# Performance work log

Hardware: AMD Instinct MI355X
Metric: run time of the kernel (lower is better)

The kernel has to match this reference:

```python
import jax, jax.numpy as jnp
import numpy as np

N_NODES = 100000
N_EDGES = 1600000
IN_CH = 32
HID = 128
OUT_CH = 32


def _glorot(key, shape):
    fan_in, fan_out = shape[1], shape[0]
    lim = (6.0 / (fan_in + fan_out)) ** 0.5
    return jax.random.uniform(key, shape, jnp.float32, -lim, lim)


def setup_inputs() -> dict:
    key = jax.random.key(0)
    ks = jax.random.split(key, 8)
    x = jax.random.normal(ks[0], (N_NODES, IN_CH), jnp.float32)
    edge_index = jax.random.randint(ks[1], (2, N_EDGES), 0, N_NODES, jnp.int64)
    # SAGEConv params: lin_l (neighbor agg, with bias), lin_r (root, no bias)
    W1_l = _glorot(ks[2], (HID, IN_CH))
    W1_r = _glorot(ks[3], (HID, IN_CH))
    b1 = jnp.zeros((HID,), jnp.float32)
    W2_l = _glorot(ks[4], (OUT_CH, HID))
    W2_r = _glorot(ks[5], (OUT_CH, HID))
    b2 = jnp.zeros((OUT_CH,), jnp.float32)
    return {"x": x, "edge_index": edge_index,
            "W1_l": W1_l, "W1_r": W1_r, "b1": b1,
            "W2_l": W2_l, "W2_r": W2_r, "b2": b2}


def _sage_conv(x, src, dst, W_l, W_r, b):
    # mean aggregation of neighbor features j -> i over edges (src=j, dst=i)
    agg = jax.ops.segment_sum(x[src], dst, num_segments=N_NODES)  # [N, C]
    deg = jax.ops.segment_sum(jnp.ones((src.shape[0],), x.dtype), dst,
                              num_segments=N_NODES)
    agg = agg / jnp.maximum(deg, 1.0)[:, None]
    return agg @ W_l.T + x @ W_r.T + b


def reference(x, edge_index, W1_l, W1_r, b1, W2_l, W2_r, b2):
    src, dst = edge_index[0], edge_index[1]
    h = _sage_conv(x, src, dst, W1_l, W1_r, b1)
    h = jax.nn.relu(h)
    # dropout is identity in eval mode (training=False)
    out = _sage_conv(h, src, dst, W2_l, W2_r, b2)
    return out
```

## Files before the change

kernel.cpp:

```cpp
#include <hip/hip_runtime.h>
#include <hip/hip_bf16.h>

typedef __hip_bfloat16 bf16;
typedef unsigned short ush;
typedef __attribute__((ext_vector_type(8))) unsigned short ush8;
typedef __attribute__((ext_vector_type(8))) short s8v;
typedef __attribute__((ext_vector_type(4))) float f4;

#define IN_CH 32
#define HID 128
#define OUT_CH 32
#define S_CAP 32
#define OVF_CAP 80000
#define NB_MAX 2048
#define SC_CHUNK 8192

__device__ __forceinline__ float bf2f(ush u) {
    return __uint_as_float(((unsigned)u) << 16);
}
__device__ __forceinline__ ush f2bf(float f) {
    __hip_bfloat16 b = __float2bfloat16(f);
    return __builtin_bit_cast(ush, b);
}
__device__ __forceinline__ float ldf(const void* __restrict__ p, size_t idx, int isbf16) {
    return isbf16 ? bf2f(((const ush*)p)[idx]) : ((const float*)p)[idx];
}
__device__ __forceinline__ int ld_edge(const int* __restrict__ ei, size_t elem, int wide) {
    return wide ? ei[2 * elem] : ei[elem];
}

__global__ void k_detect(const unsigned short* __restrict__ xraw,
                         const int* __restrict__ ei, int* __restrict__ flags) {
    __shared__ int cnt_exp, any_nz;
    if (threadIdx.x == 0) { cnt_exp = 0; any_nz = 0; }
    __syncthreads();
    int local = 0;
    for (int k = threadIdx.x; k < 4096; k += 256) {
        int e = (xraw[k] >> 7) & 0xFF;
        if (e >= 100 && e <= 140) ++local;
    }
    atomicAdd(&cnt_exp, local);
    for (int k = threadIdx.x; k < 2048; k += 256)
        if (ei[2 * k + 1] != 0) any_nz = 1;
    __syncthreads();
    if (threadIdx.x == 0) {
        flags[0] = (cnt_exp > 3500) ? 1 : 0;
        flags[1] = any_nz ? 0 : 1;
    }
}

__global__ void k_fillp(const int* __restrict__ ei, int n_edges,
                        const int* __restrict__ flags,
                        int* __restrict__ cnt, int* __restrict__ csr,
                        int* __restrict__ ovf, int* __restrict__ ovfn) {
    int e = blockIdx.x * blockDim.x + threadIdx.x;
    if (e >= n_edges) return;
    int w = flags[1];
    int d  = ld_edge(ei, (size_t)n_edges + e, w);
    int sc = ld_edge(ei, (size_t)e, w);
    int r = atomicAdd(&cnt[d], 1);
    if (r < S_CAP) {
        csr[d * S_CAP + r] = sc;
    } else {
        int o = atomicAdd(ovfn, 1);
        if (o < OVF_CAP) { ((int2*)ovf)[o] = make_int2(d, sc); }
    }
}


__global__ __launch_bounds__(256) void k_hist(
        const int* __restrict__ ei, int n_edges,
        const int* __restrict__ flags,
        int* __restrict__ hist, int NB) {
    __shared__ int hl[NB_MAX];
    int t = threadIdx.x;
    for (int k = t; k < NB; k += 256) hl[k] = 0;
    __syncthreads();
    int w = flags[1];
    int stride = gridDim.x * 256;
    for (int e = blockIdx.x * 256 + t; e < n_edges; e += stride) {
        int d = ld_edge(ei, (size_t)n_edges + e, w);
        atomicAdd(&hl[d >> 8], 1);
    }
    __syncthreads();
    for (int k = t; k < NB; k += 256)
        if (hl[k]) atomicAdd(&hist[k], hl[k]);
}

__global__ __launch_bounds__(256) void k_scan(
        const int* __restrict__ hist,
        int* __restrict__ base, int* __restrict__ cursor, int NB) {
    __shared__ int part[256];
    int t = threadIdx.x;
    int chunk = (NB + 255) / 256;
    int lo = t * chunk, hi = min(NB, (t + 1) * chunk);
    int s = 0;
    for (int k = lo; k < hi; ++k) s += hist[k];
    part[t] = s;
    __syncthreads();
    if (t == 0) {
        int r = 0;
        for (int q = 0; q < 256; ++q) { int v = part[q]; part[q] = r; r += v; }
        base[NB] = r;
    }
    __syncthreads();
    int r = part[t];
    for (int k = lo; k < hi; ++k) {
        base[k] = r; cursor[k] = r;
        r += hist[k];
    }
}

__global__ __launch_bounds__(256) void k_scatter(
        const int* __restrict__ ei, int n_edges,
        const int* __restrict__ flags,
        int* __restrict__ cursor, int* __restrict__ pairs, int NB) {
    __shared__ int cA[NB_MAX];
    __shared__ int oA[NB_MAX];
    int t = threadIdx.x;
    int w = flags[1];
    int e0 = blockIdx.x * SC_CHUNK;
    int ecnt = min(SC_CHUNK, n_edges - e0);
    if (ecnt <= 0) return;
    for (int k = t; k < NB; k += 256) cA[k] = 0;
    __syncthreads();
    for (int k = t; k < ecnt; k += 256) {
        int d = ld_edge(ei, (size_t)n_edges + e0 + k, w);
        atomicAdd(&cA[d >> 8], 1);
    }
    __syncthreads();
    for (int b = t; b < NB; b += 256) {
        int c = cA[b];
        oA[b] = c ? atomicAdd(&cursor[b], c) : 0;
        cA[b] = 0;
    }
    __syncthreads();
    for (int k = t; k < ecnt; k += 256) {
        int d  = ld_edge(ei, (size_t)n_edges + e0 + k, w);
        int sc = ld_edge(ei, (size_t)e0 + k, w);
        int b = d >> 8;
        int r = atomicAdd(&cA[b], 1);
        pairs[oA[b] + r] = sc | ((d & 255) << 24);
    }
}

__global__ __launch_bounds__(256) void k_build(
        const int* __restrict__ pairs, const int* __restrict__ base,
        int* __restrict__ cnt, int* __restrict__ csr,
        int* __restrict__ ovf, int* __restrict__ ovfn, int n_nodes) {
    __shared__ int cntL[256];
    __shared__ int im[256 * S_CAP];
    int b = blockIdx.x;
    int t = threadIdx.x;
    cntL[t] = 0;
    __syncthreads();
    int s0 = base[b], s1 = base[b + 1];
    int node0 = b << 8;
    for (int k = s0 + t; k < s1; k += 256) {
        int v = pairs[k];
        int src = v & 0x00FFFFFF;
        int ld = ((unsigned)v) >> 24;
        int r = atomicAdd(&cntL[ld], 1);
        if (r < S_CAP) {
            im[ld * S_CAP + r] = src;
        } else {
            int o = atomicAdd(ovfn, 1);
            if (o < OVF_CAP) { ((int2*)ovf)[o] = make_int2(node0 + ld, src); }
        }
    }
    __syncthreads();
    int nvalid = min(256, n_nodes - node0);
    if (t < nvalid) cnt[node0 + t] = cntL[t];
    for (int k = t; k < nvalid * S_CAP; k += 256)
        csr[(size_t)node0 * S_CAP + k] = im[k];
}

__global__ __launch_bounds__(256, 8) void k_agg1(
        const void* __restrict__ x,
        const int* __restrict__ cnt, const int* __restrict__ csr,
        const int* __restrict__ ovf, const int* __restrict__ ovfn,
        const int* __restrict__ flags,
        float* __restrict__ aggf, ush* __restrict__ aggb, int aggf32,
        int n_nodes) {
    int fb = flags[0];
    int t = threadIdx.x;
    int wave = t >> 6, lane = t & 63;
    int slot = lane >> 2;
    int chunk = lane & 3;
    int st = gridDim.x * 4 * 2;
    int i = (blockIdx.x * 4 + wave) * 2;
    if (i >= n_nodes) return;
    int idxv = csr[(size_t)i * S_CAP + lane];
    int dgv  = cnt[min(i + (lane & 1), n_nodes - 1)];
    while (i < n_nodes) {
        int inext = i + st;
        int idxv_n = 0, dgv_n = 0;
        if (inext < n_nodes) {
            idxv_n = csr[(size_t)inext * S_CAP + lane];
            dgv_n  = cnt[min(inext + (lane & 1), n_nodes - 1)];
        }
        int dg0 = __shfl(dgv, 0);
        int dg1 = __shfl(dgv, 1);
        bool has1 = (i + 1) < n_nodes;
        int lim0 = min(dg0, S_CAP);
        int lim1 = has1 ? min(dg1, S_CAP) : 0;
        int lmax = max(lim0, lim1);
        float acc0[8] = {0, 0, 0, 0, 0, 0, 0, 0};
        float acc1[8] = {0, 0, 0, 0, 0, 0, 0, 0};
        if (fb) {
            const ush* xb = (const ush*)x;
            for (int g = 0; g < lmax; g += 16) {
                int k = g + slot;
                int s0 = __shfl(idxv, k);
                int s1 = __shfl(idxv, 32 + k);
                bool ok0 = k < lim0;
                bool ok1 = k < lim1;
                ush8 v0 = *(const ush8*)(xb + (size_t)(ok0 ? s0 : i) * IN_CH + chunk * 8);
                ush8 v1 = *(const ush8*)(xb + (size_t)(ok1 ? s1 : i) * IN_CH + chunk * 8);
#pragma unroll
                for (int j = 0; j < 8; ++j) {
                    acc0[j] += ok0 ? bf2f(v0[j]) : 0.0f;
                    acc1[j] += ok1 ? bf2f(v1[j]) : 0.0f;
                }
            }
            if (dg0 > S_CAP) {
                int on = min(*ovfn, OVF_CAP);
                for (int k = 0; k < on; ++k) {
                    int2 pr = ((const int2*)ovf)[k];
                    if (pr.x == i && slot == 0) {
                        ush8 v = *(const ush8*)(xb + (size_t)pr.y * IN_CH + chunk * 8);
#pragma unroll
                        for (int j = 0; j < 8; ++j) acc0[j] += bf2f(v[j]);
                    }
                }
            }
            if (has1 && dg1 > S_CAP) {
                int on = min(*ovfn, OVF_CAP);
                for (int k = 0; k < on; ++k) {
                    int2 pr = ((const int2*)ovf)[k];
                    if (pr.x == i + 1 && slot == 0) {
                        ush8 v = *(const ush8*)(xb + (size_t)pr.y * IN_CH + chunk * 8);
#pragma unroll
                        for (int j = 0; j < 8; ++j) acc1[j] += bf2f(v[j]);
                    }
                }
            }
        } else {
            const float* xb = (const float*)x;
            for (int g = 0; g < lmax; g += 16) {
                int k = g + slot;
                int s0 = __shfl(idxv, k);
                int s1 = __shfl(idxv, 32 + k);
                bool ok0 = k < lim0;
                bool ok1 = k < lim1;
                const float* r0 = xb + (size_t)(ok0 ? s0 : i) * IN_CH + chunk * 8;
                const float* r1 = xb + (size_t)(ok1 ? s1 : i) * IN_CH + chunk * 8;
                f4 a0 = *(const f4*)r0;
                f4 a1 = *(const f4*)(r0 + 4);
                f4 b0 = *(const f4*)r1;
                f4 b1 = *(const f4*)(r1 + 4);
#pragma unroll
                for (int j = 0; j < 4; ++j) {
                    acc0[j]     += ok0 ? a0[j] : 0.0f;
                    acc0[4 + j] += ok0 ? a1[j] : 0.0f;
                    acc1[j]     += ok1 ? b0[j] : 0.0f;
                    acc1[4 + j] += ok1 ? b1[j] : 0.0f;
                }
            }
            if (dg0 > S_CAP) {
                int on = min(*ovfn, OVF_CAP);
                for (int k = 0; k < on; ++k) {
                    int2 pr = ((const int2*)ovf)[k];
                    if (pr.x == i && slot == 0) {
                        const float* rp = xb + (size_t)pr.y * IN_CH + chunk * 8;
                        f4 a0 = *(const f4*)rp;
                        f4 a1 = *(const f4*)(rp + 4);
#pragma unroll
                        for (int j = 0; j < 4; ++j) { acc0[j] += a0[j]; acc0[4 + j] += a1[j]; }
                    }
                }
            }
            if (has1 && dg1 > S_CAP) {
                int on = min(*ovfn, OVF_CAP);
                for (int k = 0; k < on; ++k) {
                    int2 pr = ((const int2*)ovf)[k];
                    if (pr.x == i + 1 && slot == 0) {
                        const float* rp = xb + (size_t)pr.y * IN_CH + chunk * 8;
                        f4 a0 = *(const f4*)rp;
                        f4 a1 = *(const f4*)(rp + 4);
#pragma unroll
                        for (int j = 0; j < 4; ++j) { acc1[j] += a0[j]; acc1[4 + j] += a1[j]; }
                    }
                }
            }
        }
#pragma unroll
        for (int j = 0; j < 8; ++j) {
            acc0[j] += __shfl_xor(acc0[j], 4);
            acc0[j] += __shfl_xor(acc0[j], 8);
            acc0[j] += __shfl_xor(acc0[j], 16);
            acc0[j] += __shfl_xor(acc0[j], 32);
            acc1[j] += __shfl_xor(acc1[j], 4);
            acc1[j] += __shfl_xor(acc1[j], 8);
            acc1[j] += __shfl_xor(acc1[j], 16);
            acc1[j] += __shfl_xor(acc1[j], 32);
        }
        if (lane < 8) {
            bool second = lane >= 4;
            if (!second || has1) {
                int node = second ? i + 1 : i;
                int dg = second ? dg1 : dg0;
                float rd = 1.0f / (float)(dg > 1 ? dg : 1);
                int c = lane & 3;
                float o[8];
#pragma unroll
                for (int j = 0; j < 8; ++j)
                    o[j] = (second ? acc1[j] : acc0[j]) * rd;
                if (aggf32) {
                    float* op = aggf + (size_t)node * IN_CH + c * 8;
                    f4 o0, o1;
#pragma unroll
                    for (int j = 0; j < 4; ++j) { o0[j] = o[j]; o1[j] = o[4 + j]; }
                    *(f4*)op = o0;
                    *(f4*)(op + 4) = o1;
                } else {
                    ush8 ov;
#pragma unroll
                    for (int j = 0; j < 8; ++j) ov[j] = f2bf(o[j]);
                    *(ush8*)(aggb + (size_t)node * IN_CH + c * 8) = ov;
                }
            }
        }
        i = inext; idxv = idxv_n; dgv = dgv_n;
    }
}

__global__ __launch_bounds__(256, 4) void k_mm1_mfma(
        const void* __restrict__ x,
        const float* __restrict__ aggf, const ush* __restrict__ aggb, int aggf32,
        const void* __restrict__ W1l, const void* __restrict__ W1r,
        const void* __restrict__ b1,
        const int* __restrict__ flags,
        ush* __restrict__ hout, int n_nodes) {
    __shared__ ush wst[HID * 64];
    int fb = flags[0];
    int t = threadIdx.x;
    for (int idx = t; idx < HID * IN_CH; idx += 256) {
        int o = idx >> 5, c = idx & 31;
        wst[o * 64 + c]      = f2bf(ldf(W1l, idx, fb));
        wst[o * 64 + 32 + c] = f2bf(ldf(W1r, idx, fb));
    }
    __syncthreads();
    int wave = t >> 6, lane = t & 63;
    int col  = lane & 15;
    int kgrp = lane >> 4;
    s8v bfr[8][2];
    float bias[8];
#pragma unroll
    for (int tt = 0; tt < 8; ++tt) {
        int o = tt * 16 + col;
#pragma unroll
        for (int q = 0; q < 2; ++q)
            bfr[tt][q] = __builtin_bit_cast(s8v, *(const ush8*)&wst[o * 64 + q * 32 + kgrp * 8]);
        bias[tt] = ldf(b1, o, fb);
    }
    int gw = blockIdx.x * 4 + wave;
    int nw = gridDim.x * 4;
    for (int n0 = gw * 16; n0 < n_nodes; n0 += nw * 16) {
        int arow = n0 + col;
        if (arow >= n_nodes) arow = n_nodes - 1;
        s8v a0;
        if (aggf32) {
            const float* ap = aggf + (size_t)arow * IN_CH + kgrp * 8;
            f4 v0 = *(const f4*)ap;
            f4 v1 = *(const f4*)(ap + 4);
            ush8 tmp;
#pragma unroll
            for (int j = 0; j < 4; ++j) { tmp[j] = f2bf(v0[j]); tmp[4 + j] = f2bf(v1[j]); }
            a0 = __builtin_bit_cast(s8v, tmp);
        } else {
            a0 = __builtin_bit_cast(s8v, *(const ush8*)(aggb + (size_t)arow * IN_CH + kgrp * 8));
        }
        s8v a1;
        if (fb) {
            a1 = __builtin_bit_cast(s8v, *(const ush8*)((const ush*)x + (size_t)arow * IN_CH + kgrp * 8));
        } else {
            const float* rp = (const float*)x + (size_t)arow * IN_CH + kgrp * 8;
            f4 v0 = *(const f4*)rp;
            f4 v1 = *(const f4*)(rp + 4);
            ush8 tmp;
#pragma unroll
            for (int j = 0; j < 4; ++j) { tmp[j] = f2bf(v0[j]); tmp[4 + j] = f2bf(v1[j]); }
            a1 = __builtin_bit_cast(s8v, tmp);
        }
        f4 acc[8];
#pragma unroll
        for (int tt = 0; tt < 8; ++tt) {
            f4 z = {0, 0, 0, 0};
            z = __builtin_amdgcn_mfma_f32_16x16x32_bf16(a0, bfr[tt][0], z, 0, 0, 0);
            z = __builtin_amdgcn_mfma_f32_16x16x32_bf16(a1, bfr[tt][1], z, 0, 0, 0);
            acc[tt] = z;
        }
#pragma unroll
        for (int r = 0; r < 4; ++r) {
            int node = n0 + kgrp * 4 + r;
            if (node < n_nodes) {
#pragma unroll
                for (int tt = 0; tt < 8; ++tt) {
                    float v = acc[tt][r] + bias[tt];
                    hout[(size_t)node * HID + tt * 16 + col] = f2bf(v > 0.0f ? v : 0.0f);
                }
            }
        }
    }
}

__global__ __launch_bounds__(256, 4) void k_g_mfma(
        ush* __restrict__ h, ush* __restrict__ gout,
        const void* __restrict__ W2l, const void* __restrict__ W2r,
        const void* __restrict__ b2,
        const int* __restrict__ flags, int n_nodes) {
    __shared__ ush wst[2 * OUT_CH * HID];
    int fb = flags[0];
    int t = threadIdx.x;
    for (int idx = t; idx < OUT_CH * HID; idx += 256) {
        wst[idx]                  = f2bf(ldf(W2l, idx, fb));
        wst[OUT_CH * HID + idx]   = f2bf(ldf(W2r, idx, fb));
    }
    __syncthreads();
    int wave = t >> 6, lane = t & 63;
    int col  = lane & 15;
    int kgrp = lane >> 4;
    s8v bfr[4][4];
#pragma unroll
    for (int tt = 0; tt < 4; ++tt) {
        int base = (tt < 2 ? 0 : OUT_CH * HID) + ((tt & 1) * 16 + col) * HID + kgrp * 8;
#pragma unroll
        for (int q = 0; q < 4; ++q)
            bfr[tt][q] = __builtin_bit_cast(s8v, *(const ush8*)&wst[base + q * 32]);
    }
    float bias0 = ldf(b2, col, fb);
    float bias1 = ldf(b2, 16 + col, fb);
    int gw = blockIdx.x * 4 + wave;
    int nw = gridDim.x * 4;
    for (int n0 = gw * 16; n0 < n_nodes; n0 += nw * 16) {
        int arow = n0 + col;
        if (arow >= n_nodes) arow = n_nodes - 1;
        const ush* hp = h + (size_t)arow * HID + kgrp * 8;
        s8v a0 = __builtin_bit_cast(s8v, *(const ush8*)(hp));
        s8v a1 = __builtin_bit_cast(s8v, *(const ush8*)(hp + 32));
        s8v a2 = __builtin_bit_cast(s8v, *(const ush8*)(hp + 64));
        s8v a3 = __builtin_bit_cast(s8v, *(const ush8*)(hp + 96));
        f4 acc0 = {0, 0, 0, 0}, acc1 = {0, 0, 0, 0}, acc2 = {0, 0, 0, 0}, acc3 = {0, 0, 0, 0};
        acc0 = __builtin_amdgcn_mfma_f32_16x16x32_bf16(a0, bfr[0][0], acc0, 0, 0, 0);
        acc0 = __builtin_amdgcn_mfma_f32_16x16x32_bf16(a1, bfr[0][1], acc0, 0, 0, 0);
        acc0 = __builtin_amdgcn_mfma_f32_16x16x32_bf16(a2, bfr[0][2], acc0, 0, 0, 0);
        acc0 = __builtin_amdgcn_mfma_f32_16x16x32_bf16(a3, bfr[0][3], acc0, 0, 0, 0);
        acc1 = __builtin_amdgcn_mfma_f32_16x16x32_bf16(a0, bfr[1][0], acc1, 0, 0, 0);
        acc1 = __builtin_amdgcn_mfma_f32_16x16x32_bf16(a1, bfr[1][1], acc1, 0, 0, 0);
        acc1 = __builtin_amdgcn_mfma_f32_16x16x32_bf16(a2, bfr[1][2], acc1, 0, 0, 0);
        acc1 = __builtin_amdgcn_mfma_f32_16x16x32_bf16(a3, bfr[1][3], acc1, 0, 0, 0);
        acc2 = __builtin_amdgcn_mfma_f32_16x16x32_bf16(a0, bfr[2][0], acc2, 0, 0, 0);
        acc2 = __builtin_amdgcn_mfma_f32_16x16x32_bf16(a1, bfr[2][1], acc2, 0, 0, 0);
        acc2 = __builtin_amdgcn_mfma_f32_16x16x32_bf16(a2, bfr[2][2], acc2, 0, 0, 0);
        acc2 = __builtin_amdgcn_mfma_f32_16x16x32_bf16(a3, bfr[2][3], acc2, 0, 0, 0);
        acc3 = __builtin_amdgcn_mfma_f32_16x16x32_bf16(a0, bfr[3][0], acc3, 0, 0, 0);
        acc3 = __builtin_amdgcn_mfma_f32_16x16x32_bf16(a1, bfr[3][1], acc3, 0, 0, 0);
        acc3 = __builtin_amdgcn_mfma_f32_16x16x32_bf16(a2, bfr[3][2], acc3, 0, 0, 0);
        acc3 = __builtin_amdgcn_mfma_f32_16x16x32_bf16(a3, bfr[3][3], acc3, 0, 0, 0);
#pragma unroll
        for (int r = 0; r < 4; ++r) {
            int node = n0 + kgrp * 4 + r;
            if (node < n_nodes) {
                gout[(size_t)node * OUT_CH + col]      = f2bf(acc0[r]);
                gout[(size_t)node * OUT_CH + 16 + col] = f2bf(acc1[r]);
                h[(size_t)node * HID + 32 + col]       = f2bf(acc2[r] + bias0);
                h[(size_t)node * HID + 48 + col]       = f2bf(acc3[r] + bias1);
            }
        }
    }
}

__global__ __launch_bounds__(256, 8) void k_l2g(
        const ush* __restrict__ gbuf, const ush* __restrict__ hs,
        const int* __restrict__ cnt, const int* __restrict__ csr,
        const int* __restrict__ ovf, const int* __restrict__ ovfn,
        const int* __restrict__ flags,
        void* __restrict__ out, int n_nodes) {
    int fb = flags[0];
    int t = threadIdx.x;
    int wave = t >> 6, lane = t & 63;
    int slot = lane >> 2;
    int chunk = lane & 3;
    int st = gridDim.x * 4 * 2;
    int i = (blockIdx.x * 4 + wave) * 2;
    if (i >= n_nodes) return;
    int idxv = csr[(size_t)i * S_CAP + lane];
    int dgv  = cnt[min(i + (lane & 1), n_nodes - 1)];
    while (i < n_nodes) {
        int inext = i + st;
        int idxv_n = 0, dgv_n = 0;
        if (inext < n_nodes) {
            idxv_n = csr[(size_t)inext * S_CAP + lane];
            dgv_n  = cnt[min(inext + (lane & 1), n_nodes - 1)];
        }
        int dg0 = __shfl(dgv, 0);
        int dg1 = __shfl(dgv, 1);
        bool has1 = (i + 1) < n_nodes;
        int lim0 = min(dg0, S_CAP);
        int lim1 = has1 ? min(dg1, S_CAP) : 0;
        int lmax = max(lim0, lim1);
        float acc0[8] = {0, 0, 0, 0, 0, 0, 0, 0};
        float acc1[8] = {0, 0, 0, 0, 0, 0, 0, 0};
        for (int g = 0; g < lmax; g += 16) {
            int k = g + slot;
            int s0 = __shfl(idxv, k);
            int s1 = __shfl(idxv, 32 + k);
            bool ok0 = k < lim0;
            bool ok1 = k < lim1;
            ush8 v0 = *(const ush8*)(gbuf + (size_t)(ok0 ? s0 : i) * OUT_CH + chunk * 8);
            ush8 v1 = *(const ush8*)(gbuf + (size_t)(ok1 ? s1 : i) * OUT_CH + chunk * 8);
#pragma unroll
            for (int j = 0; j < 8; ++j) {
                acc0[j] += ok0 ? bf2f(v0[j]) : 0.0f;
                acc1[j] += ok1 ? bf2f(v1[j]) : 0.0f;
            }
        }
        if (dg0 > S_CAP) {
            int on = min(*ovfn, OVF_CAP);
            for (int k = 0; k < on; ++k) {
                int2 pr = ((const int2*)ovf)[k];
                if (pr.x == i && slot == 0) {
                    ush8 v = *(const ush8*)(gbuf + (size_t)pr.y * OUT_CH + chunk * 8);
#pragma unroll
                    for (int j = 0; j < 8; ++j) acc0[j] += bf2f(v[j]);
                }
            }
        }
        if (has1 && dg1 > S_CAP) {
            int on = min(*ovfn, OVF_CAP);
            for (int k = 0; k < on; ++k) {
                int2 pr = ((const int2*)ovf)[k];
                if (pr.x == i + 1 && slot == 0) {
                    ush8 v = *(const ush8*)(gbuf + (size_t)pr.y * OUT_CH + chunk * 8);
#pragma unroll
                    for (int j = 0; j < 8; ++j) acc1[j] += bf2f(v[j]);
                }
            }
        }
#pragma unroll
        for (int j = 0; j < 8; ++j) {
            acc0[j] += __shfl_xor(acc0[j], 4);
            acc0[j] += __shfl_xor(acc0[j], 8);
            acc0[j] += __shfl_xor(acc0[j], 16);
            acc0[j] += __shfl_xor(acc0[j], 32);
            acc1[j] += __shfl_xor(acc1[j], 4);
            acc1[j] += __shfl_xor(acc1[j], 8);
            acc1[j] += __shfl_xor(acc1[j], 16);
            acc1[j] += __shfl_xor(acc1[j], 32);
        }
        if (lane < 8) {
            bool second = lane >= 4;
            if (!second || has1) {
                int node = second ? i + 1 : i;
                int dg = second ? dg1 : dg0;
                float rd = 1.0f / (float)(dg > 1 ? dg : 1);
                int c = lane & 3;
                ush8 selfv = *(const ush8*)(hs + (size_t)node * HID + 32 + c * 8);
                if (fb) {
                    ush8 ov;
#pragma unroll
                    for (int j = 0; j < 8; ++j) {
                        float a = second ? acc1[j] : acc0[j];
                        ov[j] = f2bf(a * rd + bf2f(selfv[j]));
                    }
                    *(ush8*)((ush*)out + (size_t)node * OUT_CH + c * 8) = ov;
                } else {
                    float* op = (float*)out + (size_t)node * OUT_CH + c * 8;
                    f4 a0, a1;
#pragma unroll
                    for (int j = 0; j < 4; ++j) {
                        float x0 = second ? acc1[j]     : acc0[j];
                        float x1 = second ? acc1[4 + j] : acc0[4 + j];
                        a0[j] = x0 * rd + bf2f(selfv[j]);
                        a1[j] = x1 * rd + bf2f(selfv[4 + j]);
                    }
                    *(f4*)op = a0;
                    *(f4*)(op + 4) = a1;
                }
            }
        }
        i = inext; idxv = idxv_n; dgv = dgv_n;
    }
}

extern "C" void kernel_launch(void* const* d_in, const int* in_sizes, int n_in,
                              void* d_out, int out_size, void* d_ws, size_t ws_size,
                              hipStream_t stream) {
    const void* x   = d_in[0];
    const int*  ei  = (const int*)d_in[1];
    const void* W1l = d_in[2];
    const void* W1r = d_in[3];
    const void* b1  = d_in[4];
    const void* W2l = d_in[5];
    const void* W2r = d_in[6];
    const void* b2  = d_in[7];

    int n_nodes = in_sizes[0] / IN_CH;
    int n_edges = in_sizes[1] / 2;

    char* ws = (char*)d_ws;
    size_t o_cnt = 256;
    size_t o_csr = (o_cnt + (size_t)n_nodes * 4 + 127) & ~(size_t)127;
    size_t o_ovf = (o_csr + ((size_t)n_nodes * S_CAP + 64) * 4 + 127) & ~(size_t)127;
    size_t o_hist = o_ovf + (size_t)OVF_CAP * 8;
    size_t o_h   = (o_hist + (size_t)(3 * (NB_MAX + 2)) * 4 + 255) & ~(size_t)255;
    size_t o_gb  = (o_h + (size_t)n_nodes * HID * 2 + 255) & ~(size_t)255;
    size_t o_ag  = (o_gb + (size_t)n_nodes * OUT_CH * 2 + 255) & ~(size_t)255;
    size_t need_f32 = o_ag + (size_t)n_nodes * IN_CH * 4;

    int* flags = (int*)ws;
    int* ovfn  = (int*)(ws + 128);
    int* cnt   = (int*)(ws + o_cnt);
    int* csr   = (int*)(ws + o_csr);
    int* ovf   = (int*)(ws + o_ovf);
    int* hist  = (int*)(ws + o_hist);
    int* base  = hist + NB_MAX;
    int* curs  = base + NB_MAX + 1;
    ush* h     = (ush*)(ws + o_h);
    int* pairs = (int*)(ws + o_h);
    ush* gbuf  = (ush*)(ws + o_gb);

    int aggf32 = (ws_size >= need_f32) ? 1 : 0;
    float* aggf = (float*)(ws + o_ag);
    ush*   aggb = gbuf;

    int NB = (n_nodes + 255) >> 8;
    int use_bucket = (NB <= NB_MAX) && (n_nodes < (1 << 24)) &&
                     ((size_t)n_edges * 4 <= (size_t)n_nodes * HID * 2) && (n_edges > 0);

    hipMemsetAsync(ws, 0, 256, stream);

    k_detect<<<1, 256, 0, stream>>>((const unsigned short*)x, ei, flags);

    if (use_bucket) {
        hipMemsetAsync(hist, 0, (size_t)NB * 4, stream);
        int nchunks = (n_edges + SC_CHUNK - 1) / SC_CHUNK;
        k_hist<<<256, 256, 0, stream>>>(ei, n_edges, flags, hist, NB);
        k_scan<<<1, 256, 0, stream>>>(hist, base, curs, NB);
        k_scatter<<<nchunks, 256, 0, stream>>>(ei, n_edges, flags, curs, pairs, NB);
        k_build<<<NB, 256, 0, stream>>>(pairs, base, cnt, csr, ovf, ovfn, n_nodes);
    } else {
        hipMemsetAsync(cnt, 0, (size_t)n_nodes * 4, stream);
        k_fillp<<<(n_edges + 255) / 256, 256, 0, stream>>>(ei, n_edges, flags, cnt, csr, ovf, ovfn);
    }

    k_agg1<<<2048, 256, 0, stream>>>(x, cnt, csr, ovf, ovfn, flags, aggf, aggb, aggf32, n_nodes);
    k_mm1_mfma<<<1024, 256, 0, stream>>>(x, aggf, aggb, aggf32, W1l, W1r, b1, flags, h, n_nodes);
    k_g_mfma<<<1024, 256, 0, stream>>>(h, gbuf, W2l, W2r, b2, flags, n_nodes);
    k_l2g<<<2048, 256, 0, stream>>>(gbuf, h, cnt, csr, ovf, ovfn, flags, d_out, n_nodes);
}
```

Baseline: 268.6 us.

## Remap gather kernels to one node per 4-lane group, sixteen nodes per wave

Both neighbour-gather kernels (layer-1 aggregation and layer-2 aggregation) now give each 4-lane group its own node instead of spreading two nodes' 32 neighbour slots across the whole wave. Each lane loads 8 CSR indices with vector loads, and lanes trade them with shuffles, so the cross-lane reduction tree over 16 slots is gone. The grid becomes one thread per node chunk instead of a grid-stride loop. This removes many shuffles and the masked-slot waste, but each wave now walks up to the largest degree among its 16 nodes sequentially, and the overflow scan runs per lane.

```diff
diff --git a/kernel.cpp b/kernel.cpp
--- a/kernel.cpp
+++ b/kernel.cpp
@@ -185,153 +185,96 @@
     int fb = flags[0];
     int t = threadIdx.x;
     int wave = t >> 6, lane = t & 63;
-    int slot = lane >> 2;
-    int chunk = lane & 3;
-    int st = gridDim.x * 4 * 2;
-    int i = (blockIdx.x * 4 + wave) * 2;
-    if (i >= n_nodes) return;
-    int idxv = csr[(size_t)i * S_CAP + lane];
-    int dgv  = cnt[min(i + (lane & 1), n_nodes - 1)];
-    while (i < n_nodes) {
-        int inext = i + st;
-        int idxv_n = 0, dgv_n = 0;
-        if (inext < n_nodes) {
-            idxv_n = csr[(size_t)inext * S_CAP + lane];
-            dgv_n  = cnt[min(inext + (lane & 1), n_nodes - 1)];
-        }
-        int dg0 = __shfl(dgv, 0);
-        int dg1 = __shfl(dgv, 1);
-        bool has1 = (i + 1) < n_nodes;
-        int lim0 = min(dg0, S_CAP);
-        int lim1 = has1 ? min(dg1, S_CAP) : 0;
-        int lmax = max(lim0, lim1);
-        float acc0[8] = {0, 0, 0, 0, 0, 0, 0, 0};
-        float acc1[8] = {0, 0, 0, 0, 0, 0, 0, 0};
-        if (fb) {
-            const ush* xb = (const ush*)x;
-            for (int g = 0; g < lmax; g += 16) {
-                int k = g + slot;
-                int s0 = __shfl(idxv, k);
-                int s1 = __shfl(idxv, 32 + k);
-                bool ok0 = k < lim0;
-                bool ok1 = k < lim1;
-                ush8 v0 = *(const ush8*)(xb + (size_t)(ok0 ? s0 : i) * IN_CH + chunk * 8);
-                ush8 v1 = *(const ush8*)(xb + (size_t)(ok1 ? s1 : i) * IN_CH + chunk * 8);
-#pragma unroll
-                for (int j = 0; j < 8; ++j) {
-                    acc0[j] += ok0 ? bf2f(v0[j]) : 0.0f;
-                    acc1[j] += ok1 ? bf2f(v1[j]) : 0.0f;
+    int g4 = lane & 60;
+    int c  = lane & 3;
+    int node = (blockIdx.x * 4 + wave) * 16 + (lane >> 2);
+    bool valid = node < n_nodes;
+    int nd = valid ? node : n_nodes - 1;
+    int dg = cnt[nd];
+    int lim = min(dg, S_CAP);
+    int idxr[8];
+    {
+        int4 i0 = *(const int4*)&csr[(size_t)nd * S_CAP + c * 8];
+        int4 i1 = *(const int4*)&csr[(size_t)nd * S_CAP + c * 8 + 4];
+        idxr[0] = i0.x; idxr[1] = i0.y; idxr[2] = i0.z; idxr[3] = i0.w;
+        idxr[4] = i1.x; idxr[5] = i1.y; idxr[6] = i1.z; idxr[7] = i1.w;
+    }
+    int lmax = lim;
+    lmax = max(lmax, __shfl_xor(lmax, 4));
+    lmax = max(lmax, __shfl_xor(lmax, 8));
+    lmax = max(lmax, __shfl_xor(lmax, 16));
+    lmax = max(lmax, __shfl_xor(lmax, 32));
+    float acc[8] = {0, 0, 0, 0, 0, 0, 0, 0};
+    if (fb) {
+        const ush* xb = (const ush*)x;
+        for (int kb = 0; kb < 4; ++kb) {
+            if (kb * 8 >= lmax) break;
+#pragma unroll
+            for (int kk = 0; kk < 8; ++kk) {
+                int src = __shfl(idxr[kk], g4 + kb);
+                if (kb * 8 + kk < lim) {
+                    ush8 v = *(const ush8*)(xb + (size_t)src * IN_CH + c * 8);
+#pragma unroll
+                    for (int j = 0; j < 8; ++j) acc[j] += bf2f(v[j]);
                 }
             }
-            if (dg0 > S_CAP) {
-                int on = min(*ovfn, OVF_CAP);
-                for (int k = 0; k < on; ++k) {
-                    int2 pr = ((const int2*)ovf)[k];
-                    if (pr.x == i && slot == 0) {
-                        ush8 v = *(const ush8*)(xb + (size_t)pr.y * IN_CH + chunk * 8);
-#pragma unroll
-                        for (int j = 0; j < 8; ++j) acc0[j] += bf2f(v[j]);
-                    }
+        }
+        if (dg > S_CAP) {
+            int on = min(*ovfn, OVF_CAP);
+            for (int k = 0; k < on; ++k) {
+                int2 pr = ((const int2*)ovf)[k];
+                if (pr.x == nd && valid) {
+                    ush8 v = *(const ush8*)(xb + (size_t)pr.y * IN_CH + c * 8);
+#pragma unroll
+                    for (int j = 0; j < 8; ++j) acc[j] += bf2f(v[j]);
                 }
             }
-            if (has1 && dg1 > S_CAP) {
-                int on = min(*ovfn, OVF_CAP);
-                for (int k = 0; k < on; ++k) {
-                    int2 pr = ((const int2*)ovf)[k];
-                    if (pr.x == i + 1 && slot == 0) {
-                        ush8 v = *(const ush8*)(xb + (size_t)pr.y * IN_CH + chunk * 8);
-#pragma unroll
-                        for (int j = 0; j < 8; ++j) acc1[j] += bf2f(v[j]);
-                    }
+        }
+    } else {
+        const float* xb = (const float*)x;
+        for (int kb = 0; kb < 4; ++kb) {
+            if (kb * 8 >= lmax) break;
+#pragma unroll
+            for (int kk = 0; kk < 8; ++kk) {
+                int src = __shfl(idxr[kk], g4 + kb);
+                if (kb * 8 + kk < lim) {
+                    const float* rp = xb + (size_t)src * IN_CH + c * 8;
+                    f4 a0 = *(const f4*)rp;
+                    f4 a1 = *(const f4*)(rp + 4);
+#pragma unroll
+                    for (int j = 0; j < 4; ++j) { acc[j] += a0[j]; acc[4 + j] += a1[j]; }
                 }
             }
+        }
+        if (dg > S_CAP) {
+            int on = min(*ovfn, OVF_CAP);
+            for (int k = 0; k < on; ++k) {
+                int2 pr = ((const int2*)ovf)[k];
+                if (pr.x == nd && valid) {
+                    const float* rp = xb + (size_t)pr.y * IN_CH + c * 8;
+                    f4 a0 = *(const f4*)rp;
+                    f4 a1 = *(const f4*)(rp + 4);
+#pragma unroll
+                    for (int j = 0; j < 4; ++j) { acc[j] += a0[j]; acc[4 + j] += a1[j]; }
+                }
+            }
+        }
+    }
+    if (valid) {
+        float rd = 1.0f / (float)(dg > 1 ? dg : 1);
+        if (aggf32) {
+            float* op = aggf + (size_t)node * IN_CH + c * 8;
+            f4 o0, o1;
+#pragma unroll
+            for (int j = 0; j < 4; ++j) { o0[j] = acc[j] * rd; o1[j] = acc[4 + j] * rd; }
+            *(f4*)op = o0;
+            *(f4*)(op + 4) = o1;
         } else {
-            const float* xb = (const float*)x;
-            for (int g = 0; g < lmax; g += 16) {
-                int k = g + slot;
-                int s0 = __shfl(idxv, k);
-                int s1 = __shfl(idxv, 32 + k);
-                bool ok0 = k < lim0;
-                bool ok1 = k < lim1;
-                const float* r0 = xb + (size_t)(ok0 ? s0 : i) * IN_CH + chunk * 8;
-                const float* r1 = xb + (size_t)(ok1 ? s1 : i) * IN_CH + chunk * 8;
-                f4 a0 = *(const f4*)r0;
-                f4 a1 = *(const f4*)(r0 + 4);
-                f4 b0 = *(const f4*)r1;
-                f4 b1 = *(const f4*)(r1 + 4);
-#pragma unroll
-                for (int j = 0; j < 4; ++j) {
-                    acc0[j]     += ok0 ? a0[j] : 0.0f;
-                    acc0[4 + j] += ok0 ? a1[j] : 0.0f;
-                    acc1[j]     += ok1 ? b0[j] : 0.0f;
-                    acc1[4 + j] += ok1 ? b1[j] : 0.0f;
-                }
-            }
-            if (dg0 > S_CAP) {
-                int on = min(*ovfn, OVF_CAP);
-                for (int k = 0; k < on; ++k) {
-                    int2 pr = ((const int2*)ovf)[k];
-                    if (pr.x == i && slot == 0) {
-                        const float* rp = xb + (size_t)pr.y * IN_CH + chunk * 8;
-                        f4 a0 = *(const f4*)rp;
-                        f4 a1 = *(const f4*)(rp + 4);
-#pragma unroll
-                        for (int j = 0; j < 4; ++j) { acc0[j] += a0[j]; acc0[4 + j] += a1[j]; }
-                    }
-                }
-            }
-            if (has1 && dg1 > S_CAP) {
-                int on = min(*ovfn, OVF_CAP);
-                for (int k = 0; k < on; ++k) {
-                    int2 pr = ((const int2*)ovf)[k];
-                    if (pr.x == i + 1 && slot == 0) {
-                        const float* rp = xb + (size_t)pr.y * IN_CH + chunk * 8;
-                        f4 a0 = *(const f4*)rp;
-                        f4 a1 = *(const f4*)(rp + 4);
-#pragma unroll
-                        for (int j = 0; j < 4; ++j) { acc1[j] += a0[j]; acc1[4 + j] += a1[j]; }
-                    }
-                }
-            }
-        }
-#pragma unroll
-        for (int j = 0; j < 8; ++j) {
-            acc0[j] += __shfl_xor(acc0[j], 4);
-            acc0[j] += __shfl_xor(acc0[j], 8);
-            acc0[j] += __shfl_xor(acc0[j], 16);
-            acc0[j] += __shfl_xor(acc0[j], 32);
-            acc1[j] += __shfl_xor(acc1[j], 4);
-            acc1[j] += __shfl_xor(acc1[j], 8);
-            acc1[j] += __shfl_xor(acc1[j], 16);
-            acc1[j] += __shfl_xor(acc1[j], 32);
-        }
-        if (lane < 8) {
-            bool second = lane >= 4;
-            if (!second || has1) {
-                int node = second ? i + 1 : i;
-                int dg = second ? dg1 : dg0;
-                float rd = 1.0f / (float)(dg > 1 ? dg : 1);
-                int c = lane & 3;
-                float o[8];
-#pragma unroll
-                for (int j = 0; j < 8; ++j)
-                    o[j] = (second ? acc1[j] : acc0[j]) * rd;
-                if (aggf32) {
-                    float* op = aggf + (size_t)node * IN_CH + c * 8;
-                    f4 o0, o1;
-#pragma unroll
-                    for (int j = 0; j < 4; ++j) { o0[j] = o[j]; o1[j] = o[4 + j]; }
-                    *(f4*)op = o0;
-                    *(f4*)(op + 4) = o1;
-                } else {
-                    ush8 ov;
-#pragma unroll
-                    for (int j = 0; j < 8; ++j) ov[j] = f2bf(o[j]);
-                    *(ush8*)(aggb + (size_t)node * IN_CH + c * 8) = ov;
-                }
-            }
-        }
-        i = inext; idxv = idxv_n; dgv = dgv_n;
+            ush8 ov;
+#pragma unroll
+            for (int j = 0; j < 8; ++j) ov[j] = f2bf(acc[j] * rd);
+            *(ush8*)(aggb + (size_t)node * IN_CH + c * 8) = ov;
+        }
     }
 }
 
@@ -490,107 +433,69 @@
     int fb = flags[0];
     int t = threadIdx.x;
     int wave = t >> 6, lane = t & 63;
-    int slot = lane >> 2;
-    int chunk = lane & 3;
-    int st = gridDim.x * 4 * 2;
-    int i = (blockIdx.x * 4 + wave) * 2;
-    if (i >= n_nodes) return;
-    int idxv = csr[(size_t)i * S_CAP + lane];
-    int dgv  = cnt[min(i + (lane & 1), n_nodes - 1)];
-    while (i < n_nodes) {
-        int inext = i + st;
-        int idxv_n = 0, dgv_n = 0;
-        if (inext < n_nodes) {
-            idxv_n = csr[(size_t)inext * S_CAP + lane];
-            dgv_n  = cnt[min(inext + (lane & 1), n_nodes - 1)];
-        }
-        int dg0 = __shfl(dgv, 0);
-        int dg1 = __shfl(dgv, 1);
-        bool has1 = (i + 1) < n_nodes;
-        int lim0 = min(dg0, S_CAP);
-        int lim1 = has1 ? min(dg1, S_CAP) : 0;
-        int lmax = max(lim0, lim1);
-        float acc0[8] = {0, 0, 0, 0, 0, 0, 0, 0};
-        float acc1[8] = {0, 0, 0, 0, 0, 0, 0, 0};
-        for (int g = 0; g < lmax; g += 16) {
-            int k = g + slot;
-            int s0 = __shfl(idxv, k);
-            int s1 = __shfl(idxv, 32 + k);
-            bool ok0 = k < lim0;
-            bool ok1 = k < lim1;
-            ush8 v0 = *(const ush8*)(gbuf + (size_t)(ok0 ? s0 : i) * OUT_CH + chunk * 8);
-            ush8 v1 = *(const ush8*)(gbuf + (size_t)(ok1 ? s1 : i) * OUT_CH + chunk * 8);
-#pragma unroll
-            for (int j = 0; j < 8; ++j) {
-                acc0[j] += ok0 ? bf2f(v0[j]) : 0.0f;
-                acc1[j] += ok1 ? bf2f(v1[j]) : 0.0f;
-            }
-        }
-        if (dg0 > S_CAP) {
-            int on = min(*ovfn, OVF_CAP);
-            for (int k = 0; k < on; ++k) {
-                int2 pr = ((const int2*)ovf)[k];
-                if (pr.x == i && slot == 0) {
-                    ush8 v = *(const ush8*)(gbuf + (size_t)pr.y * OUT_CH + chunk * 8);
-#pragma unroll
-                    for (int j = 0; j < 8; ++j) acc0[j] += bf2f(v[j]);
-                }
-            }
-        }
-        if (has1 && dg1 > S_CAP) {
-            int on = min(*ovfn, OVF_CAP);
-            for (int k = 0; k < on; ++k) {
-                int2 pr = ((const int2*)ovf)[k];
-                if (pr.x == i + 1 && slot == 0) {
-                    ush8 v = *(const ush8*)(gbuf + (size_t)pr.y * OUT_CH + chunk * 8);
-#pragma unroll
-                    for (int j = 0; j < 8; ++j) acc1[j] += bf2f(v[j]);
-                }
-            }
-        }
-#pragma unroll
-        for (int j = 0; j < 8; ++j) {
-            acc0[j] += __shfl_xor(acc0[j], 4);
-            acc0[j] += __shfl_xor(acc0[j], 8);
-            acc0[j] += __shfl_xor(acc0[j], 16);
-            acc0[j] += __shfl_xor(acc0[j], 32);
-            acc1[j] += __shfl_xor(acc1[j], 4);
-            acc1[j] += __shfl_xor(acc1[j], 8);
-            acc1[j] += __shfl_xor(acc1[j], 16);
-            acc1[j] += __shfl_xor(acc1[j], 32);
-        }
-        if (lane < 8) {
-            bool second = lane >= 4;
-            if (!second || has1) {
-                int node = second ? i + 1 : i;
-                int dg = second ? dg1 : dg0;
-                float rd = 1.0f / (float)(dg > 1 ? dg : 1);
-                int c = lane & 3;
-                ush8 selfv = *(const ush8*)(hs + (size_t)node * HID + 32 + c * 8);
-                if (fb) {
-                    ush8 ov;
-#pragma unroll
-                    for (int j = 0; j < 8; ++j) {
-                        float a = second ? acc1[j] : acc0[j];
-                        ov[j] = f2bf(a * rd + bf2f(selfv[j]));
-                    }
-                    *(ush8*)((ush*)out + (size_t)node * OUT_CH + c * 8) = ov;
-                } else {
-                    float* op = (float*)out + (size_t)node * OUT_CH + c * 8;
-                    f4 a0, a1;
-#pragma unroll
-                    for (int j = 0; j < 4; ++j) {
-                        float x0 = second ? acc1[j]     : acc0[j];
-                        float x1 = second ? acc1[4 + j] : acc0[4 + j];
-                        a0[j] = x0 * rd + bf2f(selfv[j]);
-                        a1[j] = x1 * rd + bf2f(selfv[4 + j]);
-                    }
-                    *(f4*)op = a0;
-                    *(f4*)(op + 4) = a1;
-                }
-            }
-        }
-        i = inext; idxv = idxv_n; dgv = dgv_n;
+    int g4 = lane & 60;
+    int c  = lane & 3;
+    int node = (blockIdx.x * 4 + wave) * 16 + (lane >> 2);
+    bool valid = node < n_nodes;
+    int nd = valid ? node : n_nodes - 1;
+    int dg = cnt[nd];
+    int lim = min(dg, S_CAP);
+    int idxr[8];
+    {
+        int4 i0 = *(const int4*)&csr[(size_t)nd * S_CAP + c * 8];
+        int4 i1 = *(const int4*)&csr[(size_t)nd * S_CAP + c * 8 + 4];
+        idxr[0] = i0.x; idxr[1] = i0.y; idxr[2] = i0.z; idxr[3] = i0.w;
+        idxr[4] = i1.x; idxr[5] = i1.y; idxr[6] = i1.z; idxr[7] = i1.w;
+    }
+    int lmax = lim;
+    lmax = max(lmax, __shfl_xor(lmax, 4));
+    lmax = max(lmax, __shfl_xor(lmax, 8));
+    lmax = max(lmax, __shfl_xor(lmax, 16));
+    lmax = max(lmax, __shfl_xor(lmax, 32));
+    float acc[8] = {0, 0, 0, 0, 0, 0, 0, 0};
+    for (int kb = 0; kb < 4; ++kb) {
+        if (kb * 8 >= lmax) break;
+#pragma unroll
+        for (int kk = 0; kk < 8; ++kk) {
+            int src = __shfl(idxr[kk], g4 + kb);
+            if (kb * 8 + kk < lim) {
+                ush8 v = *(const ush8*)(gbuf + (size_t)src * OUT_CH + c * 8);
+#pragma unroll
+                for (int j = 0; j < 8; ++j) acc[j] += bf2f(v[j]);
+            }
+        }
+    }
+    if (dg > S_CAP) {
+        int on = min(*ovfn, OVF_CAP);
+        for (int k = 0; k < on; ++k) {
+            int2 pr = ((const int2*)ovf)[k];
+            if (pr.x == nd && valid) {
+                ush8 v = *(const ush8*)(gbuf + (size_t)pr.y * OUT_CH + c * 8);
+#pragma unroll
+                for (int j = 0; j < 8; ++j) acc[j] += bf2f(v[j]);
+            }
+        }
+    }
+    if (valid) {
+        float rd = 1.0f / (float)(dg > 1 ? dg : 1);
+        ush8 selfv = *(const ush8*)(hs + (size_t)node * HID + 32 + c * 8);
+        if (fb) {
+            ush8 ov;
+#pragma unroll
+            for (int j = 0; j < 8; ++j)
+                ov[j] = f2bf(acc[j] * rd + bf2f(selfv[j]));
+            *(ush8*)((ush*)out + (size_t)node * OUT_CH + c * 8) = ov;
+        } else {
+            float* op = (float*)out + (size_t)node * OUT_CH + c * 8;
+            f4 a0, a1;
+#pragma unroll
+            for (int j = 0; j < 4; ++j) {
+                a0[j] = acc[j] * rd + bf2f(selfv[j]);
+                a1[j] = acc[4 + j] * rd + bf2f(selfv[4 + j]);
+            }
+            *(f4*)op = a0;
+            *(f4*)(op + 4) = a1;
+        }
     }
 }
 
@@ -655,8 +560,9 @@
         k_fillp<<<(n_edges + 255) / 256, 256, 0, stream>>>(ei, n_edges, flags, cnt, csr, ovf, ovfn);
     }
 
-    k_agg1<<<2048, 256, 0, stream>>>(x, cnt, csr, ovf, ovfn, flags, aggf, aggb, aggf32, n_nodes);
+    int nblk_g = (n_nodes + 63) / 64;
+    k_agg1<<<nblk_g, 256, 0, stream>>>(x, cnt, csr, ovf, ovfn, flags, aggf, aggb, aggf32, n_nodes);
     k_mm1_mfma<<<1024, 256, 0, stream>>>(x, aggf, aggb, aggf32, W1l, W1r, b1, flags, h, n_nodes);
     k_g_mfma<<<1024, 256, 0, stream>>>(h, gbuf, W2l, W2r, b2, flags, n_nodes);
-    k_l2g<<<2048, 256, 0, stream>>>(gbuf, h, cnt, csr, ovf, ovfn, flags, d_out, n_nodes);
-}
+    k_l2g<<<nblk_g, 256, 0, stream>>>(gbuf, h, cnt, csr, ovf, ovfn, flags, d_out, n_nodes);
+}
```

Result: faster. 233.8 us (-13.0%).
